# Kernel optimization log

Measured on AMD Instinct MI355X. Metric: run time of the kernel, lower is better.

## Reference

```python
import jax, jax.numpy as jnp
import numpy as np

HIDDEN = 2048
HEADS = 16
HEAD_DIM = HIDDEN // HEADS
ROPE_BASE = 10000.0


def apply_rope(x):
    # x: [B, H, S, d]  (Llama-style half-split RoPE)
    d = x.shape[-1]
    S = x.shape[-2]
    inv_freq = 1.0 / (ROPE_BASE ** (jnp.arange(0, d, 2, dtype=jnp.float32) / d))
    freqs = jnp.arange(S, dtype=jnp.float32)[:, None] * inv_freq[None, :]  # [S, d/2]
    cos = jnp.concatenate([jnp.cos(freqs), jnp.cos(freqs)], axis=-1)  # [S, d]
    sin = jnp.concatenate([jnp.sin(freqs), jnp.sin(freqs)], axis=-1)
    x1, x2 = jnp.split(x, 2, axis=-1)
    rot = jnp.concatenate([-x2, x1], axis=-1)
    return x * cos.astype(x.dtype) + rot * sin.astype(x.dtype)


def setup_inputs() -> dict:
    key = jax.random.key(0)
    ks = jax.random.split(key, 6)
    B, S = 4, 1024
    x = jax.random.normal(ks[0], (B, S, HIDDEN), dtype=jnp.float32)
    attention_mask = jnp.zeros((B, S), dtype=jnp.float32)  # additive mask
    scale = 1.0 / np.sqrt(HIDDEN)
    Wq = jax.random.normal(ks[1], (HIDDEN, HIDDEN), dtype=jnp.float32) * scale
    Wk = jax.random.normal(ks[2], (HIDDEN, HIDDEN), dtype=jnp.float32) * scale
    Wv = jax.random.normal(ks[3], (HIDDEN, HIDDEN), dtype=jnp.float32) * scale
    Wo = jax.random.normal(ks[4], (HIDDEN, HIDDEN), dtype=jnp.float32) * scale
    return {"x": x, "attention_mask": attention_mask, "Wq": Wq, "Wk": Wk, "Wv": Wv, "Wo": Wo}


def reference(x, attention_mask, Wq, Wk, Wv, Wo):
    B, S, D = x.shape
    H, d = HEADS, HEAD_DIM
    # projections (nn.Linear: y = x @ W.T, no bias)
    q = jnp.einsum('bsd,ed->bse', x, Wq).reshape(B, S, H, d).transpose(0, 2, 1, 3)
    k = jnp.einsum('bsd,ed->bse', x, Wk).reshape(B, S, H, d).transpose(0, 2, 1, 3)
    v = jnp.einsum('bsd,ed->bse', x, Wv).reshape(B, S, H, d).transpose(0, 2, 1, 3)
    q = apply_rope(q)
    k = apply_rope(k)
    scores = jnp.einsum('bhqd,bhkd->bhqk', q, k) / jnp.sqrt(jnp.float32(d))
    causal = jnp.where(jnp.tril(jnp.ones((S, S), dtype=bool)), 0.0, -jnp.inf).astype(scores.dtype)
    scores = scores + causal[None, None]
    scores = scores + attention_mask[:, None, None, :]
    attn_weights = jax.nn.softmax(scores, axis=-1)
    # dropout is identity in eval mode
    out = jnp.einsum('bhqk,bhkd->bhqd', attn_weights, v)
    out = out.transpose(0, 2, 1, 3).reshape(B, S, D)
    out = jnp.einsum('bsd,ed->bse', out, Wo)
    return (out, attn_weights)
```

## Files before the change

### kernel.cpp

```cpp
#include <hip/hip_runtime.h>
#include <hip/hip_bf16.h>


typedef __attribute__((ext_vector_type(8))) short bf16x8;
typedef __attribute__((ext_vector_type(4))) float f32x4;

#define GLD_LDS16(g, l)                                                      \
  __builtin_amdgcn_global_load_lds(                                          \
      (const __attribute__((address_space(1))) unsigned int*)(g),            \
      (__attribute__((address_space(3))) unsigned int*)(l), 16, 0, 0)

__global__ __launch_bounds__(256) void cast_all(
    const float* __restrict__ x, const float* __restrict__ Wq,
    const float* __restrict__ Wk, const float* __restrict__ Wv,
    const float* __restrict__ Wo, __hip_bfloat16* __restrict__ ws) {
  int idx = blockIdx.x * 256 + threadIdx.x;
  const float* src;
  __hip_bfloat16* dst;
  int off;
  if (idx < 1048576) {
    src = x; dst = ws + 4194304; off = idx;
  } else if (idx < 1572864) {
    src = Wq; dst = ws + 12582912; off = idx - 1048576;
  } else if (idx < 2097152) {
    src = Wk; dst = ws + 16777216; off = idx - 1572864;
  } else if (idx < 2621440) {
    src = Wv; dst = ws + 20971520; off = idx - 2097152;
  } else {
    src = Wo; dst = ws; off = idx - 2621440;
  }
  const float4* p = (const float4*)src;
  float4 a = p[(size_t)off * 2], b = p[(size_t)off * 2 + 1];
  __hip_bfloat16 h[8] = {__float2bfloat16(a.x), __float2bfloat16(a.y),
                         __float2bfloat16(a.z), __float2bfloat16(a.w),
                         __float2bfloat16(b.x), __float2bfloat16(b.y),
                         __float2bfloat16(b.z), __float2bfloat16(b.w)};
  uint4 u;
  __builtin_memcpy(&u, h, 16);
  ((uint4*)dst)[off] = u;
}

__global__ __launch_bounds__(256) void gemm_qkv(
    const __hip_bfloat16* __restrict__ A, const __hip_bfloat16* __restrict__ W,
    __hip_bfloat16* __restrict__ QKV, __hip_bfloat16* __restrict__ Vt) {
  __shared__ alignas(16) __hip_bfloat16 lA[128][64];
  __shared__ alignas(16) __hip_bfloat16 lB[128][64];

  const int tid = threadIdx.x;
  const int m0 = blockIdx.y * 128;
  const int n0 = blockIdx.x * 128;
  const int z = blockIdx.z;
  const __hip_bfloat16* Bm = W + (size_t)z * (2048 * 2048);

  const int lane = tid & 63;
  const int wid = tid >> 6;
  const int wm = wid * 32;
  const int frow = lane & 15;
  const int fk = (lane >> 4) * 8;

  f32x4 acc[2][8] = {};

  for (int k0 = 0; k0 < 2048; k0 += 64) {
    __syncthreads();
#pragma unroll
    for (int c = 0; c < 4; ++c) {
      int lin = c * 256 + tid;
      int r = lin >> 3;
      int col = (lin & 7) << 3;
      GLD_LDS16(A + (size_t)(m0 + r) * 2048 + k0 + col, &lA[r][col]);
    }
#pragma unroll
    for (int c = 0; c < 4; ++c) {
      int lin = c * 256 + tid;
      int r = lin >> 3;
      int col = (lin & 7) << 3;
      GLD_LDS16(Bm + (size_t)(n0 + r) * 2048 + k0 + col, &lB[r][col]);
    }
    __syncthreads();
#pragma unroll
    for (int kk = 0; kk < 64; kk += 32) {
      bf16x8 av[2], bv[8];
#pragma unroll
      for (int i = 0; i < 2; ++i)
        av[i] = *(const bf16x8*)&lA[wm + i * 16 + frow][kk + fk];
#pragma unroll
      for (int i = 0; i < 8; ++i)
        bv[i] = *(const bf16x8*)&lB[i * 16 + frow][kk + fk];
#pragma unroll
      for (int mi = 0; mi < 2; ++mi)
#pragma unroll
        for (int ni = 0; ni < 8; ++ni)
          acc[mi][ni] = __builtin_amdgcn_mfma_f32_16x16x32_bf16(
              av[mi], bv[ni], acc[mi][ni], 0, 0, 0);
    }
  }

  const int r0 = (lane >> 4) * 4;
  const int cc = lane & 15;
  __hip_bfloat16* C = QKV + (size_t)z * (4096 * 2048);

  if (z < 2) {
    float invf[4];
#pragma unroll
    for (int ni = 0; ni < 4; ++ni)
      invf[ni] = __expf(-(float)(ni * 16 + cc) * 0.143911568312128f);
#pragma unroll
    for (int mi = 0; mi < 2; ++mi) {
#pragma unroll
      for (int rr = 0; rr < 4; ++rr) {
        int m = m0 + wm + mi * 16 + r0 + rr;
        float spos = (float)(m & 1023);
        __hip_bfloat16* crow = C + (size_t)m * 2048 + n0;
#pragma unroll
        for (int ni = 0; ni < 4; ++ni) {
          float sn, c;
          __sincosf(spos * invf[ni], &sn, &c);
          float x1 = acc[mi][ni][rr], x2 = acc[mi][ni + 4][rr];
          crow[ni * 16 + cc] = __float2bfloat16(x1 * c - x2 * sn);
          crow[(ni + 4) * 16 + cc] = __float2bfloat16(x2 * c + x1 * sn);
        }
      }
    }
  } else {
    const int hh = n0 >> 7;
#pragma unroll
    for (int mi = 0; mi < 2; ++mi) {
      int m = m0 + wm + mi * 16 + r0;
      int bb = m >> 10;
      int s = m & 1023;
      __hip_bfloat16* vdst = Vt + (((size_t)bb * 16 + hh) * 128) * 1024;
#pragma unroll
      for (int ni = 0; ni < 8; ++ni) {
        int d = ni * 16 + cc;
        __hip_bfloat16 hv[4] = {__float2bfloat16(acc[mi][ni][0]),
                                __float2bfloat16(acc[mi][ni][1]),
                                __float2bfloat16(acc[mi][ni][2]),
                                __float2bfloat16(acc[mi][ni][3])};
        unsigned long long u;
        __builtin_memcpy(&u, hv, 8);
        *(unsigned long long*)&vdst[(size_t)d * 1024 + s] = u;
      }
    }
  }
}

__global__ __launch_bounds__(256) void gemm_scores(
    const __hip_bfloat16* __restrict__ Qb, const __hip_bfloat16* __restrict__ Kb,
    const float* __restrict__ mask, float* __restrict__ Cbase,
    float* __restrict__ part) {
  __shared__ alignas(16) __hip_bfloat16 lA[128][64];
  __shared__ alignas(16) __hip_bfloat16 lB[128][64];

  const int tid = threadIdx.x;
  const int m0 = blockIdx.y * 128;
  const int n0 = blockIdx.x * 128;
  if (n0 > m0) return;
  const int z = blockIdx.z;
  const int b = z >> 4, h = z & 15;
  const __hip_bfloat16* A = Qb + ((size_t)b * 1024) * 2048 + h * 128;
  const __hip_bfloat16* Bm = Kb + ((size_t)b * 1024) * 2048 + h * 128;

  const int lane = tid & 63;
  const int wid = tid >> 6;
  const int wm = (wid & 1) * 64;
  const int wn = (wid >> 1) * 64;
  const int frow = lane & 15;
  const int fk = (lane >> 4) * 8;

  f32x4 acc[4][4] = {};

  for (int k0 = 0; k0 < 128; k0 += 64) {
    __syncthreads();
#pragma unroll
    for (int c = 0; c < 4; ++c) {
      int lin = c * 256 + tid;
      int r = lin >> 3;
      int col = (lin & 7) << 3;
      GLD_LDS16(A + (size_t)(m0 + r) * 2048 + k0 + col, &lA[r][col]);
    }
#pragma unroll
    for (int c = 0; c < 4; ++c) {
      int lin = c * 256 + tid;
      int r = lin >> 3;
      int col = (lin & 7) << 3;
      GLD_LDS16(Bm + (size_t)(n0 + r) * 2048 + k0 + col, &lB[r][col]);
    }
    __syncthreads();
#pragma unroll
    for (int kk = 0; kk < 64; kk += 32) {
      bf16x8 av[4], bv[4];
#pragma unroll
      for (int i = 0; i < 4; ++i)
        av[i] = *(const bf16x8*)&lA[wm + i * 16 + frow][kk + fk];
#pragma unroll
      for (int i = 0; i < 4; ++i)
        bv[i] = *(const bf16x8*)&lB[wn + i * 16 + frow][kk + fk];
#pragma unroll
      for (int mi = 0; mi < 4; ++mi)
#pragma unroll
        for (int ni = 0; ni < 4; ++ni)
          acc[mi][ni] = __builtin_amdgcn_mfma_f32_16x16x32_bf16(
              av[mi], bv[ni], acc[mi][ni], 0, 0, 0);
    }
  }

  const int r0 = (lane >> 4) * 4;
  const int cc = lane & 15;
  const float scale = 0.08838834764831845f;
  float* C = Cbase + (size_t)z * (1024 * 1024);

#pragma unroll
  for (int mi = 0; mi < 4; ++mi)
#pragma unroll
    for (int ni = 0; ni < 4; ++ni)
#pragma unroll
      for (int r = 0; r < 4; ++r)
        C[(size_t)(m0 + wm + mi * 16 + r0 + r) * 1024 +
          (n0 + wn + ni * 16 + cc)] = acc[mi][ni][r] * scale;

  const float* mrow = mask + b * 1024;
  float mk2[4];
#pragma unroll
  for (int ni = 0; ni < 4; ++ni) mk2[ni] = mrow[n0 + wn + ni * 16 + cc];
  float2* p2 = (float2*)part +
               (((((size_t)z * 8 + blockIdx.y) * 8 + blockIdx.x) * 2 +
                 (wid >> 1))) * 128;
#pragma unroll
  for (int mi = 0; mi < 4; ++mi) {
#pragma unroll
    for (int r = 0; r < 4; ++r) {
      const int i = m0 + wm + mi * 16 + r0 + r;
      float sv[4];
      bool ok[4];
#pragma unroll
      for (int ni = 0; ni < 4; ++ni) {
        int j = n0 + wn + ni * 16 + cc;
        ok[ni] = (j <= i);
        sv[ni] = ok[ni] ? acc[mi][ni][r] * scale + mk2[ni] : -3.0e38f;
      }
      float lm = fmaxf(fmaxf(sv[0], sv[1]), fmaxf(sv[2], sv[3]));
      float ls = 0.f;
#pragma unroll
      for (int ni = 0; ni < 4; ++ni)
        ls += ok[ni] ? __expf(sv[ni] - lm) : 0.f;
#pragma unroll
      for (int off = 1; off < 16; off <<= 1) {
        float om = __shfl_xor(lm, off, 64);
        float os = __shfl_xor(ls, off, 64);
        float nm = fmaxf(lm, om);
        ls = ls * __expf(lm - nm) + os * __expf(om - nm);
        lm = nm;
      }
      if (cc == 0) p2[wm + mi * 16 + r0 + r] = float2{lm, ls};
    }
  }
}

__global__ __launch_bounds__(256) void gemm_pv(
    float* __restrict__ Sb, const __hip_bfloat16* __restrict__ Vt,
    const float* __restrict__ mask, const float* __restrict__ part,
    __hip_bfloat16* __restrict__ AO) {
  __shared__ alignas(16) __hip_bfloat16 lA[128][64];
  __shared__ alignas(16) __hip_bfloat16 lB[128][64];
  __shared__ float smx[128], sinv[128];

  const int tid = threadIdx.x;
  const int z = blockIdx.x;
  const int ytile = 7 - blockIdx.y;
  const int m0 = ytile * 128;
  const int b = z >> 4, h = z & 15;
  float* S = Sb + (size_t)z * (1024 * 1024);
  const __hip_bfloat16* Bm = Vt + (size_t)z * (128 * 1024);
  const float* mrow = mask + b * 1024;
  const int K = m0 + 128;

  if (tid < 128) {
    const float2* pp =
        (const float2*)part + ((size_t)z * 8 + ytile) * 16 * 128;
    float m = -3.0e38f, s = 0.f;
    for (int x = 0; x < 2 * (ytile + 1); ++x) {
      float2 p = pp[x * 128 + tid];
      float nm = fmaxf(m, p.x);
      s = s * __expf(m - nm) + p.y * __expf(p.x - nm);
      m = nm;
    }
    smx[tid] = m;
    sinv[tid] = 1.0f / s;
  }
  __syncthreads();

  const int sr = tid >> 4;
  const int scol = (tid & 15) << 2;
  float mx[8], inv[8];
#pragma unroll
  for (int c = 0; c < 8; ++c) {
    mx[c] = smx[c * 16 + sr];
    inv[c] = sinv[c * 16 + sr];
  }

  const int lane = tid & 63;
  const int wid = tid >> 6;
  const int wm = (wid & 1) * 64;
  const int wn = (wid >> 1) * 64;
  const int frow = lane & 15;
  const int fk = (lane >> 4) * 8;

  f32x4 acc[4][4] = {};

  for (int k0 = 0; k0 < K; k0 += 64) {
    __syncthreads();
    float4 mk = *(const float4*)&mrow[k0 + scol];
#pragma unroll
    for (int c = 0; c < 8; ++c) {
      int r = c * 16 + sr;
      int i = m0 + r;
      size_t soff = (size_t)i * 1024 + k0 + scol;
      float4 v = *(const float4*)&S[soff];
      float s[4] = {v.x + mk.x, v.y + mk.y, v.z + mk.z, v.w + mk.w};
      int j = k0 + scol;
      float w[4];
#pragma unroll
      for (int e = 0; e < 4; ++e)
        w[e] = (j + e <= i && s[e] > -1.0e38f) ? __expf(s[e] - mx[c]) * inv[c]
                                               : 0.f;
      float4 o = {w[0], w[1], w[2], w[3]};
      *(float4*)&S[soff] = o;
      __hip_bfloat16 hh[4] = {__float2bfloat16(w[0]), __float2bfloat16(w[1]),
                              __float2bfloat16(w[2]), __float2bfloat16(w[3])};
      unsigned long long u;
      __builtin_memcpy(&u, hh, 8);
      *(unsigned long long*)&lA[r][scol] = u;
    }
#pragma unroll
    for (int c = 0; c < 4; ++c) {
      int lin = c * 256 + tid;
      int r = lin >> 3;
      int col = (lin & 7) << 3;
      GLD_LDS16(Bm + (size_t)r * 1024 + k0 + col, &lB[r][col]);
    }
    __syncthreads();
#pragma unroll
    for (int kk = 0; kk < 64; kk += 32) {
      bf16x8 av[4], bv[4];
#pragma unroll
      for (int i = 0; i < 4; ++i)
        av[i] = *(const bf16x8*)&lA[wm + i * 16 + frow][kk + fk];
#pragma unroll
      for (int i = 0; i < 4; ++i)
        bv[i] = *(const bf16x8*)&lB[wn + i * 16 + frow][kk + fk];
#pragma unroll
      for (int mi = 0; mi < 4; ++mi)
#pragma unroll
        for (int ni = 0; ni < 4; ++ni)
          acc[mi][ni] = __builtin_amdgcn_mfma_f32_16x16x32_bf16(
              av[mi], bv[ni], acc[mi][ni], 0, 0, 0);
    }
  }

  const int r0 = (lane >> 4) * 4;
  const int cc = lane & 15;
  __hip_bfloat16* C = AO + ((size_t)b * 1024) * 2048 + h * 128;
#pragma unroll
  for (int mi = 0; mi < 4; ++mi)
#pragma unroll
    for (int ni = 0; ni < 4; ++ni)
#pragma unroll
      for (int r = 0; r < 4; ++r)
        C[(size_t)(m0 + wm + mi * 16 + r0 + r) * 2048 +
          (wn + ni * 16 + cc)] = __float2bfloat16(acc[mi][ni][r]);
}

__global__ __launch_bounds__(256) void gemm_out(
    const __hip_bfloat16* __restrict__ A, const __hip_bfloat16* __restrict__ Bm,
    float* __restrict__ Cbase) {
  __shared__ alignas(16) __hip_bfloat16 lA[128][64];
  __shared__ alignas(16) __hip_bfloat16 lB[128][64];

  const int tid = threadIdx.x;
  const int m0 = blockIdx.y * 128;
  const int n0 = blockIdx.x * 128;

  const int lane = tid & 63;
  const int wid = tid >> 6;
  const int wm = (wid & 1) * 64;
  const int wn = (wid >> 1) * 64;
  const int frow = lane & 15;
  const int fk = (lane >> 4) * 8;

  f32x4 acc[4][4] = {};

  for (int k0 = 0; k0 < 2048; k0 += 64) {
    __syncthreads();
#pragma unroll
    for (int c = 0; c < 4; ++c) {
      int lin = c * 256 + tid;
      int r = lin >> 3;
      int col = (lin & 7) << 3;
      GLD_LDS16(A + (size_t)(m0 + r) * 2048 + k0 + col, &lA[r][col]);
    }
#pragma unroll
    for (int c = 0; c < 4; ++c) {
      int lin = c * 256 + tid;
      int r = lin >> 3;
      int col = (lin & 7) << 3;
      GLD_LDS16(Bm + (size_t)(n0 + r) * 2048 + k0 + col, &lB[r][col]);
    }
    __syncthreads();
#pragma unroll
    for (int kk = 0; kk < 64; kk += 32) {
      bf16x8 av[4], bv[4];
#pragma unroll
      for (int i = 0; i < 4; ++i)
        av[i] = *(const bf16x8*)&lA[wm + i * 16 + frow][kk + fk];
#pragma unroll
      for (int i = 0; i < 4; ++i)
        bv[i] = *(const bf16x8*)&lB[wn + i * 16 + frow][kk + fk];
#pragma unroll
      for (int mi = 0; mi < 4; ++mi)
#pragma unroll
        for (int ni = 0; ni < 4; ++ni)
          acc[mi][ni] = __builtin_amdgcn_mfma_f32_16x16x32_bf16(
              av[mi], bv[ni], acc[mi][ni], 0, 0, 0);
    }
  }

  const int r0 = (lane >> 4) * 4;
  const int cc = lane & 15;
#pragma unroll
  for (int mi = 0; mi < 4; ++mi)
#pragma unroll
    for (int ni = 0; ni < 4; ++ni)
#pragma unroll
      for (int r = 0; r < 4; ++r)
        Cbase[(size_t)(m0 + wm + mi * 16 + r0 + r) * 2048 +
              (n0 + wn + ni * 16 + cc)] = acc[mi][ni][r];
}

extern "C" void kernel_launch(void* const* d_in, const int* in_sizes, int n_in,
                              void* d_out, int out_size, void* d_ws,
                              size_t ws_size, hipStream_t stream) {
  const float* x = (const float*)d_in[0];
  const float* mask = (const float*)d_in[1];
  const float* Wq = (const float*)d_in[2];
  const float* Wk = (const float*)d_in[3];
  const float* Wv = (const float*)d_in[4];
  const float* Wo = (const float*)d_in[5];
  float* out = (float*)d_out;
  float* attnw = out + (size_t)4 * 1024 * 2048;

  __hip_bfloat16* wsb = (__hip_bfloat16*)d_ws;
  __hip_bfloat16* Wob = wsb;
  __hip_bfloat16* xb  = wsb + 4194304;
  __hip_bfloat16* Wqb = wsb + 12582912;
  __hip_bfloat16* Qb  = wsb + 25165824;
  __hip_bfloat16* Kb  = wsb + 33554432;
  __hip_bfloat16* Vt  = wsb + 50331648;
  __hip_bfloat16* AO  = wsb + 4194304;
  float* part = (float*)(wsb + 12582912);

  cast_all<<<12288, 256, 0, stream>>>(x, Wq, Wk, Wv, Wo, wsb);
  gemm_qkv<<<dim3(16, 32, 3), 256, 0, stream>>>(xb, Wqb, Qb, Vt);
  gemm_scores<<<dim3(8, 8, 64), 256, 0, stream>>>(Qb, Kb, mask, attnw, part);
  gemm_pv<<<dim3(64, 8), 256, 0, stream>>>(attnw, Vt, mask, part, AO);
  gemm_out<<<dim3(16, 32), 256, 0, stream>>>(AO, Wob, out);
}
```

Before: 768.6 us.

## Store locally-normalized exponentials in scores pass, rescale per chunk in PV

After: 729.5 us. -5.1%, faster.

```diff
diff --git a/kernel.cpp b/kernel.cpp
--- a/kernel.cpp
+++ b/kernel.cpp
@@ -208,16 +208,6 @@
   const int cc = lane & 15;
   const float scale = 0.08838834764831845f;
   float* C = Cbase + (size_t)z * (1024 * 1024);
-
-#pragma unroll
-  for (int mi = 0; mi < 4; ++mi)
-#pragma unroll
-    for (int ni = 0; ni < 4; ++ni)
-#pragma unroll
-      for (int r = 0; r < 4; ++r)
-        C[(size_t)(m0 + wm + mi * 16 + r0 + r) * 1024 +
-          (n0 + wn + ni * 16 + cc)] = acc[mi][ni][r] * scale;
-
   const float* mrow = mask + b * 1024;
   float mk2[4];
 #pragma unroll
@@ -225,6 +215,7 @@
   float2* p2 = (float2*)part +
                (((((size_t)z * 8 + blockIdx.y) * 8 + blockIdx.x) * 2 +
                  (wid >> 1))) * 128;
+
 #pragma unroll
   for (int mi = 0; mi < 4; ++mi) {
 #pragma unroll
@@ -239,18 +230,21 @@
         sv[ni] = ok[ni] ? acc[mi][ni][r] * scale + mk2[ni] : -3.0e38f;
       }
       float lm = fmaxf(fmaxf(sv[0], sv[1]), fmaxf(sv[2], sv[3]));
+#pragma unroll
+      for (int off = 1; off < 16; off <<= 1)
+        lm = fmaxf(lm, __shfl_xor(lm, off, 64));
+      float ev[4];
       float ls = 0.f;
 #pragma unroll
-      for (int ni = 0; ni < 4; ++ni)
-        ls += ok[ni] ? __expf(sv[ni] - lm) : 0.f;
-#pragma unroll
-      for (int off = 1; off < 16; off <<= 1) {
-        float om = __shfl_xor(lm, off, 64);
-        float os = __shfl_xor(ls, off, 64);
-        float nm = fmaxf(lm, om);
-        ls = ls * __expf(lm - nm) + os * __expf(om - nm);
-        lm = nm;
+      for (int ni = 0; ni < 4; ++ni) {
+        ev[ni] = ok[ni] ? __expf(sv[ni] - lm) : 0.f;
+        ls += ev[ni];
       }
+#pragma unroll
+      for (int off = 1; off < 16; off <<= 1) ls += __shfl_xor(ls, off, 64);
+      float* crow = &C[(size_t)i * 1024 + n0 + wn + cc];
+#pragma unroll
+      for (int ni = 0; ni < 4; ++ni) crow[ni * 16] = ev[ni];
       if (cc == 0) p2[wm + mi * 16 + r0 + r] = float2{lm, ls};
     }
   }
@@ -258,11 +252,10 @@
 
 __global__ __launch_bounds__(256) void gemm_pv(
     float* __restrict__ Sb, const __hip_bfloat16* __restrict__ Vt,
-    const float* __restrict__ mask, const float* __restrict__ part,
-    __hip_bfloat16* __restrict__ AO) {
+    const float* __restrict__ part, __hip_bfloat16* __restrict__ AO) {
   __shared__ alignas(16) __hip_bfloat16 lA[128][64];
   __shared__ alignas(16) __hip_bfloat16 lB[128][64];
-  __shared__ float smx[128], sinv[128];
+  __shared__ float lfac[16][128];
 
   const int tid = threadIdx.x;
   const int z = blockIdx.x;
@@ -271,32 +264,27 @@
   const int b = z >> 4, h = z & 15;
   float* S = Sb + (size_t)z * (1024 * 1024);
   const __hip_bfloat16* Bm = Vt + (size_t)z * (128 * 1024);
-  const float* mrow = mask + b * 1024;
   const int K = m0 + 128;
+  const int nx = 2 * (ytile + 1);
 
   if (tid < 128) {
     const float2* pp =
         (const float2*)part + ((size_t)z * 8 + ytile) * 16 * 128;
     float m = -3.0e38f, s = 0.f;
-    for (int x = 0; x < 2 * (ytile + 1); ++x) {
+    for (int x = 0; x < nx; ++x) {
       float2 p = pp[x * 128 + tid];
       float nm = fmaxf(m, p.x);
       s = s * __expf(m - nm) + p.y * __expf(p.x - nm);
       m = nm;
     }
-    smx[tid] = m;
-    sinv[tid] = 1.0f / s;
+    float iv = 1.0f / s;
+    for (int x = 0; x < nx; ++x)
+      lfac[x][tid] = __expf(pp[x * 128 + tid].x - m) * iv;
   }
   __syncthreads();
 
   const int sr = tid >> 4;
   const int scol = (tid & 15) << 2;
-  float mx[8], inv[8];
-#pragma unroll
-  for (int c = 0; c < 8; ++c) {
-    mx[c] = smx[c * 16 + sr];
-    inv[c] = sinv[c * 16 + sr];
-  }
 
   const int lane = tid & 63;
   const int wid = tid >> 6;
@@ -309,24 +297,17 @@
 
   for (int k0 = 0; k0 < K; k0 += 64) {
     __syncthreads();
-    float4 mk = *(const float4*)&mrow[k0 + scol];
+    const int xk = k0 >> 6;
 #pragma unroll
     for (int c = 0; c < 8; ++c) {
       int r = c * 16 + sr;
-      int i = m0 + r;
-      size_t soff = (size_t)i * 1024 + k0 + scol;
+      size_t soff = (size_t)(m0 + r) * 1024 + k0 + scol;
       float4 v = *(const float4*)&S[soff];
-      float s[4] = {v.x + mk.x, v.y + mk.y, v.z + mk.z, v.w + mk.w};
-      int j = k0 + scol;
-      float w[4];
-#pragma unroll
-      for (int e = 0; e < 4; ++e)
-        w[e] = (j + e <= i && s[e] > -1.0e38f) ? __expf(s[e] - mx[c]) * inv[c]
-                                               : 0.f;
-      float4 o = {w[0], w[1], w[2], w[3]};
+      float fc = lfac[xk][r];
+      float4 o = {v.x * fc, v.y * fc, v.z * fc, v.w * fc};
       *(float4*)&S[soff] = o;
-      __hip_bfloat16 hh[4] = {__float2bfloat16(w[0]), __float2bfloat16(w[1]),
-                              __float2bfloat16(w[2]), __float2bfloat16(w[3])};
+      __hip_bfloat16 hh[4] = {__float2bfloat16(o.x), __float2bfloat16(o.y),
+                              __float2bfloat16(o.z), __float2bfloat16(o.w)};
       unsigned long long u;
       __builtin_memcpy(&u, hh, 8);
       *(unsigned long long*)&lA[r][scol] = u;
@@ -461,6 +442,6 @@
   cast_all<<<12288, 256, 0, stream>>>(x, Wq, Wk, Wv, Wo, wsb);
   gemm_qkv<<<dim3(16, 32, 3), 256, 0, stream>>>(xb, Wqb, Qb, Vt);
   gemm_scores<<<dim3(8, 8, 64), 256, 0, stream>>>(Qb, Kb, mask, attnw, part);
-  gemm_pv<<<dim3(64, 8), 256, 0, stream>>>(attnw, Vt, mask, part, AO);
+  gemm_pv<<<dim3(64, 8), 256, 0, stream>>>(attnw, Vt, part, AO);
   gemm_out<<<dim3(16, 32), 256, 0, stream>>>(AO, Wob, out);
 }
```

## Precompute softmax row stats in separate QK pass, write final weights directly

Applied to the files above, without the earlier changes.

New measurement: 682.5 us. 11.2% less time.

```diff
diff --git a/kernel.cpp b/kernel.cpp
--- a/kernel.cpp
+++ b/kernel.cpp
@@ -144,21 +144,155 @@
   }
 }
 
+__global__ __launch_bounds__(256) void qk_stats(
+    const __hip_bfloat16* __restrict__ Qb, const __hip_bfloat16* __restrict__ Kb,
+    const float* __restrict__ mask, float* __restrict__ pstat) {
+  __shared__ alignas(16) __hip_bfloat16 lK[64][128];
+
+  const int tid = threadIdx.x;
+  const int z = blockIdx.y;
+  int bx = blockIdx.x;
+  int my = 0;
+  for (; my < 8; ++my) {
+    int n = (my >> 1) + 1;
+    if (bx < n) break;
+    bx -= n;
+  }
+  const int chunk = bx;
+  const int m0 = my * 128;
+  const int b = z >> 4, h = z & 15;
+  const int kbeg = chunk * 256;
+  const int kend = (kbeg + 256 < m0 + 128) ? (kbeg + 256) : (m0 + 128);
+
+  const int lane = tid & 63;
+  const int wid = tid >> 6;
+  const int wm = wid * 32;
+  const int frow = lane & 15;
+  const int fk = (lane >> 4) * 8;
+  const int r0 = (lane >> 4) * 4;
+  const int cc = lane & 15;
+
+  const __hip_bfloat16* Qh = Qb + ((size_t)b * 1024) * 2048 + h * 128;
+  const __hip_bfloat16* Kh = Kb + ((size_t)b * 1024) * 2048 + h * 128;
+  const float* mrow = mask + b * 1024;
+  const float scale = 0.08838834764831845f;
+
+  bf16x8 qf[2][4];
+#pragma unroll
+  for (int mi = 0; mi < 2; ++mi)
+#pragma unroll
+    for (int kq = 0; kq < 4; ++kq)
+      qf[mi][kq] = *(const bf16x8*)
+          &Qh[(size_t)(m0 + wm + mi * 16 + frow) * 2048 + kq * 32 + fk];
+
+  float mx[2][4], sm[2][4];
+#pragma unroll
+  for (int mi = 0; mi < 2; ++mi)
+#pragma unroll
+    for (int rr = 0; rr < 4; ++rr) { mx[mi][rr] = -3.0e38f; sm[mi][rr] = 0.f; }
+
+  for (int j0 = kbeg; j0 < kend; j0 += 64) {
+    __syncthreads();
+#pragma unroll
+    for (int c = 0; c < 4; ++c) {
+      int lin = c * 256 + tid;
+      int r = lin >> 4;
+      int col = (lin & 15) << 3;
+      GLD_LDS16(Kh + (size_t)(j0 + r) * 2048 + col, &lK[r][col]);
+    }
+    __syncthreads();
+    f32x4 as[2][4] = {};
+#pragma unroll
+    for (int kq = 0; kq < 4; ++kq) {
+      bf16x8 bk[4];
+#pragma unroll
+      for (int ni = 0; ni < 4; ++ni)
+        bk[ni] = *(const bf16x8*)&lK[ni * 16 + frow][kq * 32 + fk];
+#pragma unroll
+      for (int mi = 0; mi < 2; ++mi)
+#pragma unroll
+        for (int ni = 0; ni < 4; ++ni)
+          as[mi][ni] = __builtin_amdgcn_mfma_f32_16x16x32_bf16(
+              qf[mi][kq], bk[ni], as[mi][ni], 0, 0, 0);
+    }
+    float mk[4];
+#pragma unroll
+    for (int ni = 0; ni < 4; ++ni) mk[ni] = mrow[j0 + ni * 16 + cc];
+#pragma unroll
+    for (int mi = 0; mi < 2; ++mi) {
+#pragma unroll
+      for (int rr = 0; rr < 4; ++rr) {
+        const int i = m0 + wm + mi * 16 + r0 + rr;
+        float sv[4];
+        bool ok[4];
+#pragma unroll
+        for (int ni = 0; ni < 4; ++ni) {
+          int j = j0 + ni * 16 + cc;
+          ok[ni] = (j <= i);
+          sv[ni] = ok[ni] ? as[mi][ni][rr] * scale + mk[ni] : -3.0e38f;
+        }
+        float tm = fmaxf(fmaxf(sv[0], sv[1]), fmaxf(sv[2], sv[3]));
+        if (tm > mx[mi][rr]) {
+          sm[mi][rr] *= __expf(mx[mi][rr] - tm);
+          mx[mi][rr] = tm;
+        }
+#pragma unroll
+        for (int ni = 0; ni < 4; ++ni)
+          sm[mi][rr] += ok[ni] ? __expf(sv[ni] - mx[mi][rr]) : 0.f;
+      }
+    }
+  }
+
+  float2* p2 = (float2*)pstat + (((size_t)z * 8 + my) * 4 + chunk) * 128;
+#pragma unroll
+  for (int mi = 0; mi < 2; ++mi) {
+#pragma unroll
+    for (int rr = 0; rr < 4; ++rr) {
+#pragma unroll
+      for (int off = 1; off < 16; off <<= 1) {
+        float om = __shfl_xor(mx[mi][rr], off, 64);
+        float os = __shfl_xor(sm[mi][rr], off, 64);
+        float nm = fmaxf(mx[mi][rr], om);
+        sm[mi][rr] = sm[mi][rr] * __expf(mx[mi][rr] - nm) + os * __expf(om - nm);
+        mx[mi][rr] = nm;
+      }
+      if (cc == 0)
+        p2[wm + mi * 16 + r0 + rr] = float2{mx[mi][rr], sm[mi][rr]};
+    }
+  }
+}
+
 __global__ __launch_bounds__(256) void gemm_scores(
     const __hip_bfloat16* __restrict__ Qb, const __hip_bfloat16* __restrict__ Kb,
     const float* __restrict__ mask, float* __restrict__ Cbase,
-    float* __restrict__ part) {
+    const float* __restrict__ pstat) {
   __shared__ alignas(16) __hip_bfloat16 lA[128][64];
   __shared__ alignas(16) __hip_bfloat16 lB[128][64];
+  __shared__ float smx[128], sinv[128];
 
   const int tid = threadIdx.x;
   const int m0 = blockIdx.y * 128;
   const int n0 = blockIdx.x * 128;
   if (n0 > m0) return;
   const int z = blockIdx.z;
+  const int my = blockIdx.y;
   const int b = z >> 4, h = z & 15;
   const __hip_bfloat16* A = Qb + ((size_t)b * 1024) * 2048 + h * 128;
   const __hip_bfloat16* Bm = Kb + ((size_t)b * 1024) * 2048 + h * 128;
+
+  if (tid < 128) {
+    const float2* pp = (const float2*)pstat + ((size_t)z * 8 + my) * 4 * 128;
+    int nc = (my >> 1) + 1;
+    float m = -3.0e38f, s = 0.f;
+    for (int c = 0; c < nc; ++c) {
+      float2 p = pp[c * 128 + tid];
+      float nm = fmaxf(m, p.x);
+      s = s * __expf(m - nm) + p.y * __expf(p.x - nm);
+      m = nm;
+    }
+    smx[tid] = m;
+    sinv[tid] = 1.0f / s;
+  }
 
   const int lane = tid & 63;
   const int wid = tid >> 6;
@@ -208,95 +342,49 @@
   const int cc = lane & 15;
   const float scale = 0.08838834764831845f;
   float* C = Cbase + (size_t)z * (1024 * 1024);
-
-#pragma unroll
-  for (int mi = 0; mi < 4; ++mi)
-#pragma unroll
-    for (int ni = 0; ni < 4; ++ni)
-#pragma unroll
-      for (int r = 0; r < 4; ++r)
-        C[(size_t)(m0 + wm + mi * 16 + r0 + r) * 1024 +
-          (n0 + wn + ni * 16 + cc)] = acc[mi][ni][r] * scale;
-
   const float* mrow = mask + b * 1024;
   float mk2[4];
 #pragma unroll
   for (int ni = 0; ni < 4; ++ni) mk2[ni] = mrow[n0 + wn + ni * 16 + cc];
-  float2* p2 = (float2*)part +
-               (((((size_t)z * 8 + blockIdx.y) * 8 + blockIdx.x) * 2 +
-                 (wid >> 1))) * 128;
+
 #pragma unroll
   for (int mi = 0; mi < 4; ++mi) {
 #pragma unroll
     for (int r = 0; r < 4; ++r) {
-      const int i = m0 + wm + mi * 16 + r0 + r;
-      float sv[4];
-      bool ok[4];
+      const int rl = wm + mi * 16 + r0 + r;
+      const int i = m0 + rl;
+      const float mxv = smx[rl];
+      const float iv = sinv[rl];
+      float* crow = &C[(size_t)i * 1024 + n0 + wn + cc];
 #pragma unroll
       for (int ni = 0; ni < 4; ++ni) {
         int j = n0 + wn + ni * 16 + cc;
-        ok[ni] = (j <= i);
-        sv[ni] = ok[ni] ? acc[mi][ni][r] * scale + mk2[ni] : -3.0e38f;
+        float w = (j <= i)
+                      ? __expf(acc[mi][ni][r] * scale + mk2[ni] - mxv) * iv
+                      : 0.f;
+        crow[ni * 16] = w;
       }
-      float lm = fmaxf(fmaxf(sv[0], sv[1]), fmaxf(sv[2], sv[3]));
-      float ls = 0.f;
-#pragma unroll
-      for (int ni = 0; ni < 4; ++ni)
-        ls += ok[ni] ? __expf(sv[ni] - lm) : 0.f;
-#pragma unroll
-      for (int off = 1; off < 16; off <<= 1) {
-        float om = __shfl_xor(lm, off, 64);
-        float os = __shfl_xor(ls, off, 64);
-        float nm = fmaxf(lm, om);
-        ls = ls * __expf(lm - nm) + os * __expf(om - nm);
-        lm = nm;
-      }
-      if (cc == 0) p2[wm + mi * 16 + r0 + r] = float2{lm, ls};
     }
   }
 }
 
 __global__ __launch_bounds__(256) void gemm_pv(
-    float* __restrict__ Sb, const __hip_bfloat16* __restrict__ Vt,
-    const float* __restrict__ mask, const float* __restrict__ part,
+    const float* __restrict__ Sb, const __hip_bfloat16* __restrict__ Vt,
     __hip_bfloat16* __restrict__ AO) {
   __shared__ alignas(16) __hip_bfloat16 lA[128][64];
   __shared__ alignas(16) __hip_bfloat16 lB[128][64];
-  __shared__ float smx[128], sinv[128];
 
   const int tid = threadIdx.x;
   const int z = blockIdx.x;
   const int ytile = 7 - blockIdx.y;
   const int m0 = ytile * 128;
   const int b = z >> 4, h = z & 15;
-  float* S = Sb + (size_t)z * (1024 * 1024);
+  const float* S = Sb + (size_t)z * (1024 * 1024);
   const __hip_bfloat16* Bm = Vt + (size_t)z * (128 * 1024);
-  const float* mrow = mask + b * 1024;
   const int K = m0 + 128;
-
-  if (tid < 128) {
-    const float2* pp =
-        (const float2*)part + ((size_t)z * 8 + ytile) * 16 * 128;
-    float m = -3.0e38f, s = 0.f;
-    for (int x = 0; x < 2 * (ytile + 1); ++x) {
-      float2 p = pp[x * 128 + tid];
-      float nm = fmaxf(m, p.x);
-      s = s * __expf(m - nm) + p.y * __expf(p.x - nm);
-      m = nm;
-    }
-    smx[tid] = m;
-    sinv[tid] = 1.0f / s;
-  }
-  __syncthreads();
 
   const int sr = tid >> 4;
   const int scol = (tid & 15) << 2;
-  float mx[8], inv[8];
-#pragma unroll
-  for (int c = 0; c < 8; ++c) {
-    mx[c] = smx[c * 16 + sr];
-    inv[c] = sinv[c * 16 + sr];
-  }
 
   const int lane = tid & 63;
   const int wid = tid >> 6;
@@ -309,24 +397,12 @@
 
   for (int k0 = 0; k0 < K; k0 += 64) {
     __syncthreads();
-    float4 mk = *(const float4*)&mrow[k0 + scol];
 #pragma unroll
     for (int c = 0; c < 8; ++c) {
       int r = c * 16 + sr;
-      int i = m0 + r;
-      size_t soff = (size_t)i * 1024 + k0 + scol;
-      float4 v = *(const float4*)&S[soff];
-      float s[4] = {v.x + mk.x, v.y + mk.y, v.z + mk.z, v.w + mk.w};
-      int j = k0 + scol;
-      float w[4];
-#pragma unroll
-      for (int e = 0; e < 4; ++e)
-        w[e] = (j + e <= i && s[e] > -1.0e38f) ? __expf(s[e] - mx[c]) * inv[c]
-                                               : 0.f;
-      float4 o = {w[0], w[1], w[2], w[3]};
-      *(float4*)&S[soff] = o;
-      __hip_bfloat16 hh[4] = {__float2bfloat16(w[0]), __float2bfloat16(w[1]),
-                              __float2bfloat16(w[2]), __float2bfloat16(w[3])};
+      float4 v = *(const float4*)&S[(size_t)(m0 + r) * 1024 + k0 + scol];
+      __hip_bfloat16 hh[4] = {__float2bfloat16(v.x), __float2bfloat16(v.y),
+                              __float2bfloat16(v.z), __float2bfloat16(v.w)};
       unsigned long long u;
       __builtin_memcpy(&u, hh, 8);
       *(unsigned long long*)&lA[r][scol] = u;
@@ -456,11 +532,12 @@
   __hip_bfloat16* Kb  = wsb + 33554432;
   __hip_bfloat16* Vt  = wsb + 50331648;
   __hip_bfloat16* AO  = wsb + 4194304;
-  float* part = (float*)(wsb + 12582912);
+  float* pstat = (float*)(wsb + 12582912);
 
   cast_all<<<12288, 256, 0, stream>>>(x, Wq, Wk, Wv, Wo, wsb);
   gemm_qkv<<<dim3(16, 32, 3), 256, 0, stream>>>(xb, Wqb, Qb, Vt);
-  gemm_scores<<<dim3(8, 8, 64), 256, 0, stream>>>(Qb, Kb, mask, attnw, part);
-  gemm_pv<<<dim3(64, 8), 256, 0, stream>>>(attnw, Vt, mask, part, AO);
+  qk_stats<<<dim3(20, 64), 256, 0, stream>>>(Qb, Kb, mask, pstat);
+  gemm_scores<<<dim3(8, 8, 64), 256, 0, stream>>>(Qb, Kb, mask, attnw, pstat);
+  gemm_pv<<<dim3(64, 8), 256, 0, stream>>>(attnw, Vt, AO);
   gemm_out<<<dim3(16, 32), 256, 0, stream>>>(AO, Wob, out);
 }
```
